# Kernel optimization log

Hardware: AMD Instinct MI355X
Metric: run time of the kernel (lower is better)

## Reference

```python
import jax, jax.numpy as jnp
import numpy as np

B, J, FIN, FOUT = 8192, 17, 128, 128
BN_EPS = 1e-5


def setup_inputs() -> dict:
    key = jax.random.key(0)
    k_x, k_w, k_adj, k_b = jax.random.split(key, 4)
    x = jax.random.normal(k_x, (B, J, FIN), dtype=jnp.float32)
    # Xavier-uniform-ish init for W [2, FIN, FOUT]
    limit = 1.414 * np.sqrt(6.0 / (FIN + FOUT))
    W = jax.random.uniform(k_w, (2, FIN, FOUT), minval=-limit, maxval=limit, dtype=jnp.float32)
    M = jnp.ones((J, FOUT), dtype=jnp.float32)
    # binary-ish skeleton adjacency buffer (constant)
    adj = (jax.random.uniform(k_adj, (J, J)) > 0.7).astype(jnp.float32)
    adj = adj + jnp.eye(J, dtype=jnp.float32)  # self loops like skeleton graphs
    adj2 = jnp.full((J, J), 1e-6, dtype=jnp.float32)
    stdv = 1.0 / np.sqrt(FOUT)
    bias = jax.random.uniform(k_b, (FOUT,), minval=-stdv, maxval=stdv, dtype=jnp.float32)
    gamma = jnp.ones((FOUT,), dtype=jnp.float32)
    beta = jnp.zeros((FOUT,), dtype=jnp.float32)
    return {"x": x, "W": W, "M": M, "adj": adj, "adj2": adj2,
            "bias": bias, "gamma": gamma, "beta": beta}


def reference(x, W, M, adj, adj2, bias, gamma, beta):
    # ModulatedGraphConv
    h0 = jnp.einsum('bjf,fo->bjo', x, W[0])
    h1 = jnp.einsum('bjf,fo->bjo', x, W[1])
    a = adj + adj2
    a = (a.T + a) * 0.5                       # symmetrize [J, J]
    diag = jnp.diagonal(a)                    # [J]
    off = a * (1.0 - jnp.eye(a.shape[0], dtype=a.dtype))  # zero diagonal
    # diag part: adj*E is diagonal -> per-node scaling; off-diag: dense matmul over J
    out = diag[None, :, None] * (M * h0) + jnp.einsum('ij,bjo->bio', off, M * h1)
    out = out + bias[None, None, :]           # [B, J, FOUT]
    # BatchNorm1d over channel dim (training-mode batch stats over B and J)
    mean = out.mean(axis=(0, 1))
    var = out.var(axis=(0, 1))                # biased variance, as torch BN uses
    out = (out - mean) * jax.lax.rsqrt(var + BN_EPS) * gamma + beta
    return jax.nn.relu(out)
```

## Files before the change

### kernel.cpp

```cpp
#include <hip/hip_runtime.h>


#define NSLOT      128
#define OFF_PART   0
#define OFF_STATS  32768
#define OFF_OFFSYM 33024
#define OFF_DIAG   33364
#define OFF_WBT    33408
#define OFF_PRE    49792
#define PRE_SHORTS (139264ull * 128ull)

typedef __attribute__((ext_vector_type(8))) short bf16x8;
typedef __attribute__((ext_vector_type(4))) short bf16x4;
typedef __attribute__((ext_vector_type(4))) float f32x4;
typedef union { unsigned u[2]; bf16x4 v; } pk4U;

__device__ __forceinline__ short f2bf(float f) {
    unsigned u = __float_as_uint(f);
    u += 0x7FFFu + ((u >> 16) & 1u);
    return (short)(u >> 16);
}
__device__ __forceinline__ float bf2f(short h) {
    return __uint_as_float(((unsigned)(unsigned short)h) << 16);
}
__device__ __forceinline__ float bflo(int p) {
    return __uint_as_float(((unsigned)p) << 16);
}
__device__ __forceinline__ float bfhi(int p) {
    return __uint_as_float(((unsigned)p) & 0xFFFF0000u);
}
__device__ __forceinline__ unsigned pk2(float a, float b) {
    unsigned r;
    asm("v_cvt_pk_bf16_f32 %0, %1, %2" : "=v"(r) : "v"(a), "v"(b));
    return r;
}

__global__ __launch_bounds__(256) void prep_kernel(
    const float* __restrict__ W, const float* __restrict__ adj,
    const float* __restrict__ adj2, float* __restrict__ wsf)
{
    const int t = threadIdx.x, b = blockIdx.x;
    if (b == 0) {
        for (int e = t; e < 340; e += 256) {
            int i = e / 20, j = e % 20;
            float v = 0.f;
            if (j < 17) {
                v = 0.5f * (adj[i*17+j] + adj2[i*17+j] + adj[j*17+i] + adj2[j*17+i]);
                if (i == j) { wsf[OFF_DIAG + i] = v; v = 0.f; }
            }
            wsf[OFF_OFFSYM + e] = v;
        }
        return;
    }
    short* wbt = (short*)(wsf + OFF_WBT);
    const int col = (b - 1) * 16 + (t >> 4);
    const int k0  = (t & 15) * 8;
    const int sel = col >> 7, colp = col & 127;
    const float* src = W + sel * 16384 + colp;
    bf16x8 p;
    #pragma unroll
    for (int e = 0; e < 8; ++e) p[e] = f2bf(src[(k0 + e) * 128]);
    *(bf16x8*)(wbt + col * 128 + k0) = p;
}

__global__ __launch_bounds__(512, 6) void conv_kernel(
    const float* __restrict__ x, const float* __restrict__ M,
    const float* __restrict__ bias, float* ws, short* __restrict__ pre)
{
    __shared__ int U[8704];
    __shared__ __align__(16) float Mlds[2176];
    __shared__ __align__(16) float offs[340];
    __shared__ float dlds[20];
    short (*A)[136] = (short(*)[136])U;

    const int tid = threadIdx.x;
    const int w = tid >> 6, l = tid & 63, c = l & 15, g = l >> 4;
    const int col = w * 16 + c;

    const float bv = bias[col];

    for (int e = tid; e < 340; e += 512) offs[e] = ws[OFF_OFFSYM + e];
    if (tid < 17) dlds[tid] = ws[OFF_DIAG + tid];
    {
        const float4* m4 = (const float4*)M;
        for (int e = tid; e < 544; e += 512)
            *(float4*)&Mlds[e * 4] = m4[e];
    }

    const float4* xsrc = (const float4*)(x + (size_t)blockIdx.x * (68 * 128));
    #pragma unroll
    for (int it = 0; it < 5; ++it) {
        int f = tid + it * 512;
        if (f < 2176) {
            float4 v = xsrc[f];
            int r = f >> 5, k0 = (f & 31) << 2;
            pk4U p;
            p.u[0] = pk2(v.x, v.y);
            p.u[1] = pk2(v.z, v.w);
            *(bf16x4*)&A[r][k0] = p.v;
        }
    }
    __syncthreads();

    const short* wbt = (const short*)(ws + OFF_WBT);
    f32x4 acc0[5], acc1[5];
    #pragma unroll
    for (int mt = 0; mt < 5; ++mt) {
        acc0[mt] = (f32x4){0.f, 0.f, 0.f, 0.f};
        acc1[mt] = (f32x4){0.f, 0.f, 0.f, 0.f};
    }
    #pragma unroll
    for (int ks = 0; ks < 4; ++ks) {
        bf16x8 b0 = *(const bf16x8*)(wbt + col * 128 + ks * 32 + g * 8);
        bf16x8 b1 = *(const bf16x8*)(wbt + (col + 128) * 128 + ks * 32 + g * 8);
        #pragma unroll
        for (int mt = 0; mt < 5; ++mt) {
            const int arow = (mt < 4) ? (mt * 16 + c) : (64 + (c & 3));
            bf16x8 af = *(const bf16x8*)&A[arow][ks * 32 + g * 8];
            acc0[mt] = __builtin_amdgcn_mfma_f32_16x16x32_bf16(af, b0, acc0[mt], 0, 0, 0);
            acc1[mt] = __builtin_amdgcn_mfma_f32_16x16x32_bf16(af, b1, acc1[mt], 0, 0, 0);
        }
    }
    __syncthreads();

    int* hw = U + w * 1088;
    #pragma unroll
    for (int mt = 0; mt < 5; ++mt) {
        #pragma unroll
        for (int r = 0; r < 4; ++r) {
            int row = mt * 16 + g * 4 + r;
            if (row < 68) {
                unsigned pk = ((unsigned)(unsigned short)f2bf(acc0[mt][r])) |
                              (((unsigned)(unsigned short)f2bf(acc1[mt][r])) << 16);
                hw[row * 16 + c] = (int)pk;
            }
        }
    }

    int pj[17]; float mcol[17];
    #pragma unroll
    for (int i = 0; i < 17; ++i) {
        pj[i]   = hw[(g * 17 + i) * 16 + c];
        mcol[i] = Mlds[i * 128 + col];
    }

    float vout[17];
    #pragma unroll
    for (int i = 0; i < 17; ++i)
        vout[i] = fmaf(dlds[i] * mcol[i], bflo(pj[i]), bv);
    #pragma unroll
    for (int j = 0; j < 17; ++j) {
        float hv = mcol[j] * bfhi(pj[j]);
        const f32x4* orow = (const f32x4*)&offs[j * 20];
        f32x4 o0 = orow[0], o1 = orow[1], o2 = orow[2], o3 = orow[3];
        float oz = offs[j * 20 + 16];
        vout[0]  = fmaf(o0.x, hv, vout[0]);
        vout[1]  = fmaf(o0.y, hv, vout[1]);
        vout[2]  = fmaf(o0.z, hv, vout[2]);
        vout[3]  = fmaf(o0.w, hv, vout[3]);
        vout[4]  = fmaf(o1.x, hv, vout[4]);
        vout[5]  = fmaf(o1.y, hv, vout[5]);
        vout[6]  = fmaf(o1.z, hv, vout[6]);
        vout[7]  = fmaf(o1.w, hv, vout[7]);
        vout[8]  = fmaf(o2.x, hv, vout[8]);
        vout[9]  = fmaf(o2.y, hv, vout[9]);
        vout[10] = fmaf(o2.z, hv, vout[10]);
        vout[11] = fmaf(o2.w, hv, vout[11]);
        vout[12] = fmaf(o3.x, hv, vout[12]);
        vout[13] = fmaf(o3.y, hv, vout[13]);
        vout[14] = fmaf(o3.z, hv, vout[14]);
        vout[15] = fmaf(o3.w, hv, vout[15]);
        vout[16] = fmaf(oz,   hv, vout[16]);
    }

    float s = 0.f, s2 = 0.f;
    const size_t gbase = ((size_t)blockIdx.x * 68 + g * 17) * 128 + col;
    #pragma unroll
    for (int i = 0; i < 17; ++i) {
        float v = vout[i];
        pre[gbase + (size_t)i * 128] = (short)pk2(v, v);
        s += v; s2 = fmaf(v, v, s2);
    }

    s  += __shfl_xor(s, 16);  s  += __shfl_xor(s, 32);
    s2 += __shfl_xor(s2, 16); s2 += __shfl_xor(s2, 32);
    if (l < 16) {
        float* slot = ws + OFF_PART + ((blockIdx.x & (NSLOT - 1)) << 8);
        atomicAdd(slot + col, s);
        atomicAdd(slot + 128 + col, s2);
    }
}

__global__ __launch_bounds__(512, 4) void conv_f32_kernel(
    const float* __restrict__ x, const float* __restrict__ M,
    const float* __restrict__ bias, float* ws, float* __restrict__ out)
{
    __shared__ int hhI[68 * 130];
    __shared__ __align__(16) float offs[340];
    short (*A)[136] = (short(*)[136])hhI;
    const int tid = threadIdx.x;
    const int w = tid >> 6, l = tid & 63, c = l & 15, g = l >> 4;
    for (int e = tid; e < 340; e += 512) offs[e] = ws[OFF_OFFSYM + e];
    const float4* xsrc = (const float4*)(x + (size_t)blockIdx.x * (68 * 128));
    #pragma unroll
    for (int it = 0; it < 5; ++it) {
        int f = tid + it * 512;
        if (f < 2176) {
            float4 v = xsrc[f];
            int r = f >> 5, k0 = (f & 31) << 2;
            pk4U p; p.u[0] = pk2(v.x, v.y); p.u[1] = pk2(v.z, v.w);
            *(bf16x4*)&A[r][k0] = p.v;
        }
    }
    if (tid < 408) { bf16x4 z = {0,0,0,0}; ((bf16x4*)&A[68][0])[tid] = z; }
    __syncthreads();
    const short* wbt = (const short*)(ws + OFF_WBT);
    const int col = w * 16 + c;
    f32x4 acc0[5], acc1[5];
    #pragma unroll
    for (int mt = 0; mt < 5; ++mt) {
        acc0[mt] = (f32x4){0.f,0.f,0.f,0.f}; acc1[mt] = (f32x4){0.f,0.f,0.f,0.f};
    }
    #pragma unroll
    for (int ks = 0; ks < 4; ++ks) {
        bf16x8 b0 = *(const bf16x8*)(wbt + col * 128 + ks * 32 + g * 8);
        bf16x8 b1 = *(const bf16x8*)(wbt + (col + 128) * 128 + ks * 32 + g * 8);
        #pragma unroll
        for (int mt = 0; mt < 5; ++mt) {
            bf16x8 af = *(const bf16x8*)&A[mt * 16 + c][ks * 32 + g * 8];
            acc0[mt] = __builtin_amdgcn_mfma_f32_16x16x32_bf16(af, b0, acc0[mt], 0, 0, 0);
            acc1[mt] = __builtin_amdgcn_mfma_f32_16x16x32_bf16(af, b1, acc1[mt], 0, 0, 0);
        }
    }
    __syncthreads();
    const float bv = bias[col];
    #pragma unroll
    for (int mt = 0; mt < 5; ++mt) {
        #pragma unroll
        for (int r = 0; r < 4; ++r) {
            int row = mt * 16 + g * 4 + r;
            if (row < 68) {
                int j = row - 17 * ((row * 241) >> 12);
                float m  = M[j * 128 + col];
                float dg = ws[OFF_DIAG + j];
                float lo = fmaf(dg * m, acc0[mt][r], bv);
                float hi = m * acc1[mt][r];
                hhI[row * 130 + col] = (int)pk2(lo, hi);
            }
        }
    }
    __syncthreads();
    const int bb = tid >> 7, o = tid & 127;
    const int rb = bb * 17;
    int pj[17];
    #pragma unroll
    for (int i = 0; i < 17; ++i) pj[i] = hhI[(rb + i) * 130 + o];
    float vout[17];
    #pragma unroll
    for (int q = 0; q < 17; ++q) vout[q] = bflo(pj[q]);
    #pragma unroll
    for (int j = 0; j < 17; ++j) {
        float h1v = bfhi(pj[j]);
        #pragma unroll
        for (int q = 0; q < 17; ++q) vout[q] = fmaf(offs[j * 20 + q], h1v, vout[q]);
    }
    float s = 0.f, s2 = 0.f;
    const size_t gbase = ((size_t)blockIdx.x * 68 + rb) * 128 + o;
    #pragma unroll
    for (int q = 0; q < 17; ++q) {
        float v = vout[q];
        out[gbase + (size_t)q * 128] = v;
        s += v; s2 = fmaf(v, v, s2);
    }
    float* slot = ws + OFF_PART + ((blockIdx.x & (NSLOT - 1)) << 8);
    atomicAdd(slot + o, s);
    atomicAdd(slot + 128 + o, s2);
}

__global__ __launch_bounds__(256) void bn_reduce_kernel(
    const float* __restrict__ part, const float* __restrict__ gamma,
    const float* __restrict__ beta, float* __restrict__ stats)
{
    const int t = threadIdx.x;
    float s = 0.f;
    #pragma unroll 8
    for (int i = 0; i < NSLOT; ++i) s += part[i * 256 + t];
    __shared__ float tot[256];
    tot[t] = s;
    __syncthreads();
    if (t < 128) {
        const float n = 139264.f;
        float mean = tot[t] / n;
        float var  = tot[t + 128] / n - mean * mean;
        var = fmaxf(var, 0.f);
        float inv = rsqrtf(var + 1e-5f);
        float sc = gamma[t] * inv;
        stats[t] = sc;
        stats[t + 128] = beta[t] - mean * sc;
    }
}

__global__ __launch_bounds__(256) void apply_bf16_kernel(
    const short* __restrict__ pre, const float* __restrict__ stats,
    float* __restrict__ out)
{
    const int tid = blockIdx.x * 256 + threadIdx.x;
    const int c0 = (tid << 3) & 127;
    float sc[8], sh[8];
    #pragma unroll
    for (int e = 0; e < 8; ++e) { sc[e] = stats[c0 + e]; sh[e] = stats[128 + c0 + e]; }
    const bf16x8* p8 = (const bf16x8*)pre;
    for (int q = tid; q < 2228224; q += 524288) {
        bf16x8 v = p8[q];
        float4 o0, o1;
        o0.x = fmaxf(fmaf(bf2f(v[0]), sc[0], sh[0]), 0.f);
        o0.y = fmaxf(fmaf(bf2f(v[1]), sc[1], sh[1]), 0.f);
        o0.z = fmaxf(fmaf(bf2f(v[2]), sc[2], sh[2]), 0.f);
        o0.w = fmaxf(fmaf(bf2f(v[3]), sc[3], sh[3]), 0.f);
        o1.x = fmaxf(fmaf(bf2f(v[4]), sc[4], sh[4]), 0.f);
        o1.y = fmaxf(fmaf(bf2f(v[5]), sc[5], sh[5]), 0.f);
        o1.z = fmaxf(fmaf(bf2f(v[6]), sc[6], sh[6]), 0.f);
        o1.w = fmaxf(fmaf(bf2f(v[7]), sc[7], sh[7]), 0.f);
        float4* dst = (float4*)(out + (size_t)q * 8);
        dst[0] = o0; dst[1] = o1;
    }
}

__global__ __launch_bounds__(256) void apply_kernel(
    float* __restrict__ out, const float* __restrict__ stats, int n4)
{
    const int tid = blockIdx.x * 256 + threadIdx.x;
    const int c0 = (tid << 2) & 127;
    const float sc0 = stats[c0],     sc1 = stats[c0 + 1],
                sc2 = stats[c0 + 2], sc3 = stats[c0 + 3];
    const float sh0 = stats[128 + c0],     sh1 = stats[128 + c0 + 1],
                sh2 = stats[128 + c0 + 2], sh3 = stats[128 + c0 + 3];
    float4* o4 = (float4*)out;
    for (int q = tid; q < n4; q += 2048 * 256) {
        float4 v = o4[q];
        v.x = fmaxf(fmaf(v.x, sc0, sh0), 0.f);
        v.y = fmaxf(fmaf(v.y, sc1, sh1), 0.f);
        v.z = fmaxf(fmaf(v.z, sc2, sh2), 0.f);
        v.w = fmaxf(fmaf(v.w, sc3, sh3), 0.f);
        o4[q] = v;
    }
}

extern "C" void kernel_launch(void* const* d_in, const int* in_sizes, int n_in,
                              void* d_out, int out_size, void* d_ws, size_t ws_size,
                              hipStream_t stream) {
    (void)in_sizes; (void)n_in; (void)out_size;
    const float* x     = (const float*)d_in[0];
    const float* W     = (const float*)d_in[1];
    const float* M     = (const float*)d_in[2];
    const float* adj   = (const float*)d_in[3];
    const float* adj2  = (const float*)d_in[4];
    const float* bias  = (const float*)d_in[5];
    const float* gamma = (const float*)d_in[6];
    const float* beta  = (const float*)d_in[7];
    float* out = (float*)d_out;
    float* wsf = (float*)d_ws;
    short* pre = (short*)(wsf + OFF_PRE);

    const bool big = ws_size >= (size_t)OFF_PRE * 4 + PRE_SHORTS * 2;

    (void)hipMemsetAsync(d_ws, 0, NSLOT * 256 * sizeof(float), stream);
    prep_kernel<<<17, 256, 0, stream>>>(W, adj, adj2, wsf);
    if (big) {
        conv_kernel<<<2048, 512, 0, stream>>>(x, M, bias, wsf, pre);
        bn_reduce_kernel<<<1, 256, 0, stream>>>(wsf + OFF_PART, gamma, beta, wsf + OFF_STATS);
        apply_bf16_kernel<<<2048, 256, 0, stream>>>(pre, wsf + OFF_STATS, out);
    } else {
        conv_f32_kernel<<<2048, 512, 0, stream>>>(x, M, bias, wsf, out);
        bn_reduce_kernel<<<1, 256, 0, stream>>>(wsf + OFF_PART, gamma, beta, wsf + OFF_STATS);
        apply_kernel<<<2048, 256, 0, stream>>>(out, wsf + OFF_STATS, 4456448);
    }
}
```

Baseline: 74.01 us.

## Process two tiles per block and prefetch next x tile into registers

Each conv block now handles two 68-row tiles, launching half as many blocks. The next tile's x data is loaded into registers while the current tile's epilogue runs, and A and the h scratch buffer get separate shared arrays so the overlap is legal. Setup work (M, offs, bias loads) is amortised over both tiles. The cost is more shared memory and register pressure: launch bounds drop from 6 to 4 blocks per CU, and the grid shrinks to 1024 blocks.

```diff
diff --git a/kernel.cpp b/kernel.cpp
--- a/kernel.cpp
+++ b/kernel.cpp
@@ -9,6 +9,7 @@
 #define OFF_WBT    33408
 #define OFF_PRE    49792
 #define PRE_SHORTS (139264ull * 128ull)
+#define TILES      2
 
 typedef __attribute__((ext_vector_type(8))) short bf16x8;
 typedef __attribute__((ext_vector_type(4))) short bf16x4;
@@ -63,21 +64,29 @@
     *(bf16x8*)(wbt + col * 128 + k0) = p;
 }
 
-__global__ __launch_bounds__(512, 6) void conv_kernel(
+__global__ __launch_bounds__(512, 4) void conv_kernel(
     const float* __restrict__ x, const float* __restrict__ M,
     const float* __restrict__ bias, float* ws, short* __restrict__ pre)
 {
-    __shared__ int U[8704];
+    __shared__ short A[68][136];
+    __shared__ int HH[8704];
     __shared__ __align__(16) float Mlds[2176];
     __shared__ __align__(16) float offs[340];
     __shared__ float dlds[20];
-    short (*A)[136] = (short(*)[136])U;
 
     const int tid = threadIdx.x;
     const int w = tid >> 6, l = tid & 63, c = l & 15, g = l >> 4;
     const int col = w * 16 + c;
+    const int tile0 = blockIdx.x * TILES;
 
     const float bv = bias[col];
+
+    float4 rv0, rv1, rv2, rv3, rv4 = {0.f, 0.f, 0.f, 0.f};
+    {
+        const float4* xs = (const float4*)(x + (size_t)tile0 * (68 * 128));
+        rv0 = xs[tid]; rv1 = xs[tid + 512]; rv2 = xs[tid + 1024]; rv3 = xs[tid + 1536];
+        if (tid < 128) rv4 = xs[tid + 2048];
+    }
 
     for (int e = tid; e < 340; e += 512) offs[e] = ws[OFF_OFFSYM + e];
     if (tid < 17) dlds[tid] = ws[OFF_DIAG + tid];
@@ -87,107 +96,124 @@
             *(float4*)&Mlds[e * 4] = m4[e];
     }
 
-    const float4* xsrc = (const float4*)(x + (size_t)blockIdx.x * (68 * 128));
-    #pragma unroll
-    for (int it = 0; it < 5; ++it) {
-        int f = tid + it * 512;
-        if (f < 2176) {
-            float4 v = xsrc[f];
-            int r = f >> 5, k0 = (f & 31) << 2;
-            pk4U p;
-            p.u[0] = pk2(v.x, v.y);
-            p.u[1] = pk2(v.z, v.w);
-            *(bf16x4*)&A[r][k0] = p.v;
-        }
-    }
-    __syncthreads();
-
     const short* wbt = (const short*)(ws + OFF_WBT);
-    f32x4 acc0[5], acc1[5];
-    #pragma unroll
-    for (int mt = 0; mt < 5; ++mt) {
-        acc0[mt] = (f32x4){0.f, 0.f, 0.f, 0.f};
-        acc1[mt] = (f32x4){0.f, 0.f, 0.f, 0.f};
-    }
-    #pragma unroll
-    for (int ks = 0; ks < 4; ++ks) {
-        bf16x8 b0 = *(const bf16x8*)(wbt + col * 128 + ks * 32 + g * 8);
-        bf16x8 b1 = *(const bf16x8*)(wbt + (col + 128) * 128 + ks * 32 + g * 8);
+    float mcol[17];
+    bool mld = false;
+
+    #pragma unroll 1
+    for (int t = 0; t < TILES; ++t) {
+        {
+            pk4U p; int f;
+            f = tid;        p.u[0] = pk2(rv0.x, rv0.y); p.u[1] = pk2(rv0.z, rv0.w);
+                            *(bf16x4*)&A[f >> 5][(f & 31) << 2] = p.v;
+            f = tid + 512;  p.u[0] = pk2(rv1.x, rv1.y); p.u[1] = pk2(rv1.z, rv1.w);
+                            *(bf16x4*)&A[f >> 5][(f & 31) << 2] = p.v;
+            f = tid + 1024; p.u[0] = pk2(rv2.x, rv2.y); p.u[1] = pk2(rv2.z, rv2.w);
+                            *(bf16x4*)&A[f >> 5][(f & 31) << 2] = p.v;
+            f = tid + 1536; p.u[0] = pk2(rv3.x, rv3.y); p.u[1] = pk2(rv3.z, rv3.w);
+                            *(bf16x4*)&A[f >> 5][(f & 31) << 2] = p.v;
+            if (tid < 128) {
+                f = tid + 2048;
+                p.u[0] = pk2(rv4.x, rv4.y); p.u[1] = pk2(rv4.z, rv4.w);
+                *(bf16x4*)&A[f >> 5][(f & 31) << 2] = p.v;
+            }
+        }
+        __syncthreads();
+
+        f32x4 acc0[5], acc1[5];
         #pragma unroll
         for (int mt = 0; mt < 5; ++mt) {
-            const int arow = (mt < 4) ? (mt * 16 + c) : (64 + (c & 3));
-            bf16x8 af = *(const bf16x8*)&A[arow][ks * 32 + g * 8];
-            acc0[mt] = __builtin_amdgcn_mfma_f32_16x16x32_bf16(af, b0, acc0[mt], 0, 0, 0);
-            acc1[mt] = __builtin_amdgcn_mfma_f32_16x16x32_bf16(af, b1, acc1[mt], 0, 0, 0);
-        }
-    }
-    __syncthreads();
-
-    int* hw = U + w * 1088;
-    #pragma unroll
-    for (int mt = 0; mt < 5; ++mt) {
-        #pragma unroll
-        for (int r = 0; r < 4; ++r) {
-            int row = mt * 16 + g * 4 + r;
-            if (row < 68) {
-                unsigned pk = ((unsigned)(unsigned short)f2bf(acc0[mt][r])) |
-                              (((unsigned)(unsigned short)f2bf(acc1[mt][r])) << 16);
-                hw[row * 16 + c] = (int)pk;
+            acc0[mt] = (f32x4){0.f, 0.f, 0.f, 0.f};
+            acc1[mt] = (f32x4){0.f, 0.f, 0.f, 0.f};
+        }
+        #pragma unroll
+        for (int ks = 0; ks < 4; ++ks) {
+            bf16x8 b0 = *(const bf16x8*)(wbt + col * 128 + ks * 32 + g * 8);
+            bf16x8 b1 = *(const bf16x8*)(wbt + (col + 128) * 128 + ks * 32 + g * 8);
+            #pragma unroll
+            for (int mt = 0; mt < 5; ++mt) {
+                const int arow = (mt < 4) ? (mt * 16 + c) : (64 + (c & 3));
+                bf16x8 af = *(const bf16x8*)&A[arow][ks * 32 + g * 8];
+                acc0[mt] = __builtin_amdgcn_mfma_f32_16x16x32_bf16(af, b0, acc0[mt], 0, 0, 0);
+                acc1[mt] = __builtin_amdgcn_mfma_f32_16x16x32_bf16(af, b1, acc1[mt], 0, 0, 0);
             }
         }
-    }
-
-    int pj[17]; float mcol[17];
-    #pragma unroll
-    for (int i = 0; i < 17; ++i) {
-        pj[i]   = hw[(g * 17 + i) * 16 + c];
-        mcol[i] = Mlds[i * 128 + col];
-    }
-
-    float vout[17];
-    #pragma unroll
-    for (int i = 0; i < 17; ++i)
-        vout[i] = fmaf(dlds[i] * mcol[i], bflo(pj[i]), bv);
-    #pragma unroll
-    for (int j = 0; j < 17; ++j) {
-        float hv = mcol[j] * bfhi(pj[j]);
-        const f32x4* orow = (const f32x4*)&offs[j * 20];
-        f32x4 o0 = orow[0], o1 = orow[1], o2 = orow[2], o3 = orow[3];
-        float oz = offs[j * 20 + 16];
-        vout[0]  = fmaf(o0.x, hv, vout[0]);
-        vout[1]  = fmaf(o0.y, hv, vout[1]);
-        vout[2]  = fmaf(o0.z, hv, vout[2]);
-        vout[3]  = fmaf(o0.w, hv, vout[3]);
-        vout[4]  = fmaf(o1.x, hv, vout[4]);
-        vout[5]  = fmaf(o1.y, hv, vout[5]);
-        vout[6]  = fmaf(o1.z, hv, vout[6]);
-        vout[7]  = fmaf(o1.w, hv, vout[7]);
-        vout[8]  = fmaf(o2.x, hv, vout[8]);
-        vout[9]  = fmaf(o2.y, hv, vout[9]);
-        vout[10] = fmaf(o2.z, hv, vout[10]);
-        vout[11] = fmaf(o2.w, hv, vout[11]);
-        vout[12] = fmaf(o3.x, hv, vout[12]);
-        vout[13] = fmaf(o3.y, hv, vout[13]);
-        vout[14] = fmaf(o3.z, hv, vout[14]);
-        vout[15] = fmaf(o3.w, hv, vout[15]);
-        vout[16] = fmaf(oz,   hv, vout[16]);
-    }
-
-    float s = 0.f, s2 = 0.f;
-    const size_t gbase = ((size_t)blockIdx.x * 68 + g * 17) * 128 + col;
-    #pragma unroll
-    for (int i = 0; i < 17; ++i) {
-        float v = vout[i];
-        pre[gbase + (size_t)i * 128] = (short)pk2(v, v);
-        s += v; s2 = fmaf(v, v, s2);
-    }
-
-    s  += __shfl_xor(s, 16);  s  += __shfl_xor(s, 32);
-    s2 += __shfl_xor(s2, 16); s2 += __shfl_xor(s2, 32);
-    if (l < 16) {
-        float* slot = ws + OFF_PART + ((blockIdx.x & (NSLOT - 1)) << 8);
-        atomicAdd(slot + col, s);
-        atomicAdd(slot + 128 + col, s2);
+        __syncthreads();
+
+        if (t + 1 < TILES) {
+            const float4* xs = (const float4*)(x + (size_t)(tile0 + t + 1) * (68 * 128));
+            rv0 = xs[tid]; rv1 = xs[tid + 512]; rv2 = xs[tid + 1024]; rv3 = xs[tid + 1536];
+            if (tid < 128) rv4 = xs[tid + 2048];
+        }
+
+        int* hw = HH + w * 1088;
+        #pragma unroll
+        for (int mt = 0; mt < 5; ++mt) {
+            #pragma unroll
+            for (int r = 0; r < 4; ++r) {
+                int row = mt * 16 + g * 4 + r;
+                if (row < 68) {
+                    unsigned pk = ((unsigned)(unsigned short)f2bf(acc0[mt][r])) |
+                                  (((unsigned)(unsigned short)f2bf(acc1[mt][r])) << 16);
+                    hw[row * 16 + c] = (int)pk;
+                }
+            }
+        }
+
+        int pj[17];
+        #pragma unroll
+        for (int i = 0; i < 17; ++i) pj[i] = hw[(g * 17 + i) * 16 + c];
+        if (!mld) {
+            #pragma unroll
+            for (int i = 0; i < 17; ++i) mcol[i] = Mlds[i * 128 + col];
+            mld = true;
+        }
+
+        float vout[17];
+        #pragma unroll
+        for (int i = 0; i < 17; ++i)
+            vout[i] = fmaf(dlds[i] * mcol[i], bflo(pj[i]), bv);
+        #pragma unroll
+        for (int j = 0; j < 17; ++j) {
+            float hv = mcol[j] * bfhi(pj[j]);
+            const f32x4* orow = (const f32x4*)&offs[j * 20];
+            f32x4 o0 = orow[0], o1 = orow[1], o2 = orow[2], o3 = orow[3];
+            float oz = offs[j * 20 + 16];
+            vout[0]  = fmaf(o0.x, hv, vout[0]);
+            vout[1]  = fmaf(o0.y, hv, vout[1]);
+            vout[2]  = fmaf(o0.z, hv, vout[2]);
+            vout[3]  = fmaf(o0.w, hv, vout[3]);
+            vout[4]  = fmaf(o1.x, hv, vout[4]);
+            vout[5]  = fmaf(o1.y, hv, vout[5]);
+            vout[6]  = fmaf(o1.z, hv, vout[6]);
+            vout[7]  = fmaf(o1.w, hv, vout[7]);
+            vout[8]  = fmaf(o2.x, hv, vout[8]);
+            vout[9]  = fmaf(o2.y, hv, vout[9]);
+            vout[10] = fmaf(o2.z, hv, vout[10]);
+            vout[11] = fmaf(o2.w, hv, vout[11]);
+            vout[12] = fmaf(o3.x, hv, vout[12]);
+            vout[13] = fmaf(o3.y, hv, vout[13]);
+            vout[14] = fmaf(o3.z, hv, vout[14]);
+            vout[15] = fmaf(o3.w, hv, vout[15]);
+            vout[16] = fmaf(oz,   hv, vout[16]);
+        }
+
+        float s = 0.f, s2 = 0.f;
+        const size_t gbase = ((size_t)(tile0 + t) * 68 + g * 17) * 128 + col;
+        #pragma unroll
+        for (int i = 0; i < 17; ++i) {
+            float v = vout[i];
+            pre[gbase + (size_t)i * 128] = (short)pk2(v, v);
+            s += v; s2 = fmaf(v, v, s2);
+        }
+
+        s  += __shfl_xor(s, 16);  s  += __shfl_xor(s, 32);
+        s2 += __shfl_xor(s2, 16); s2 += __shfl_xor(s2, 32);
+        if (l < 16) {
+            float* slot = ws + OFF_PART + (((tile0 + t) & (NSLOT - 1)) << 8);
+            atomicAdd(slot + col, s);
+            atomicAdd(slot + 128 + col, s2);
+        }
     }
 }
 
@@ -367,7 +393,7 @@
     (void)hipMemsetAsync(d_ws, 0, NSLOT * 256 * sizeof(float), stream);
     prep_kernel<<<17, 256, 0, stream>>>(W, adj, adj2, wsf);
     if (big) {
-        conv_kernel<<<2048, 512, 0, stream>>>(x, M, bias, wsf, pre);
+        conv_kernel<<<1024, 512, 0, stream>>>(x, M, bias, wsf, pre);
         bn_reduce_kernel<<<1, 256, 0, stream>>>(wsf + OFF_PART, gamma, beta, wsf + OFF_STATS);
         apply_bf16_kernel<<<2048, 256, 0, stream>>>(pre, wsf + OFF_STATS, out);
     } else {
```

Result: slower. 78.25 us (+5.7%).
